# Optimization experiments

Measured on AMD Instinct MI355X. Metric: run time of the kernel, lower is better.

## Reference

```python
import jax, jax.numpy as jnp
import numpy as np

B, D, M_CONS = 512, 1024, 256
TOL = 0.01          # projection_tolerance
ROUNDS = 3
RHO0 = 3.0          # step
XRHO0 = 0.5         # forward() default xrho
FACTOR = 1.0
MAX_ITER = 30       # cap on the (originally unbounded) Dykstra while-loop


def setup_inputs() -> dict:
    key = jax.random.key(0)
    k1, k2, k3, k4, k5 = jax.random.split(key, 5)
    A = jax.random.normal(k1, (M_CONS, D), jnp.float32) / np.float32(np.sqrt(D))
    # feasible b so the polyhedron {Ax=b, x>=0} is nonempty and Dykstra converges
    x_feas = jax.nn.relu(jax.random.normal(k2, (D,), jnp.float32))
    b = A @ x_feas                                  # [M_CONS]
    AA = A.T @ jnp.linalg.inv(A @ A.T)              # [D, M_CONS], precomputed as in __init__
    c = jax.random.normal(k3, (B, D), jnp.float32)
    L = jax.random.normal(k4, (D, D), jnp.float32)
    Lam = 1.0 + 0.1 * jax.random.normal(k5, (D,), jnp.float32)
    return {"c": c, "A": A, "b": b, "AA": AA, "L": L, "Lam": Lam}


def reference(c, A, b, AA, L, Lam):
    # step matrix: L @ diag(Lam) @ inv(L)   (recomputed identically each round in torch)
    M = (L * Lam[None, :]) @ jnp.linalg.inv(L)      # [D, D]

    def proj(x):  # affine projection onto {Ax = b}: (x.T - AA @ (A x.T - b)).T
        return x - (x @ A.T - b[None, :]) @ AA.T    # [B, D]

    def project_pol(x0):  # Dykstra alternating projection onto {Ax=b} n {x>=0}
        def body(carry, _):
            x, p, q, y_out, done = carry
            y = proj(x + p)
            err = jnp.max(jax.nn.relu(-y))
            y_out = jnp.where(done, y_out, y)       # freeze output at first convergence
            xn = jax.nn.relu(y + q)
            pn = x + p - y
            qn = y + q - xn
            sel = lambda old, new: jnp.where(done, old, new)
            new_done = done | (err < TOL)
            return (sel(x, xn), sel(p, pn), sel(q, qn), y_out, new_done), None

        z = jnp.zeros_like(x0)
        init = (x0, z, z, x0, jnp.array(False))
        (xf, pf, qf, y_out, d), _ = jax.lax.scan(body, init, None, length=MAX_ITER)
        return y_out

    x = jnp.zeros_like(c)
    rho, xrho = RHO0, XRHO0
    for _ in range(ROUNDS):
        x = x - (xrho * (x @ M.T) + rho * c)
        x = project_pol(x)
        rho = rho * FACTOR
        xrho = xrho * FACTOR
    return x
```

## Files before the change

kernel.cpp:

```cpp
#include <hip/hip_runtime.h>

#define D      1024
#define BSZ    512
#define MC     256
#define NBK    64
#define NPAN   16
#define N_ROUNDS 3
#define MAXIT  30
#define TOLV   0.01f
#define RHOV   3.0f
#define XRHOV  0.5f
#define GRID   256
#define NGA    128
#define NGB    128

#define TS   0
#define QS   4096
#define US   8192
#define PART 9216
#define BS   13312
#define RED  13568
#define SMF  13600

struct KArgs {
  const float *c, *A, *b, *AA, *L, *Lam;
  float *yout, *F, *Ybuf, *Wm;
  float *t, *err, *At, *AAt;
  int *perm, *rmap;
  unsigned *slotsF, *slotsG;
};

__device__ __forceinline__ void fbar(unsigned* slots, int lid, int count, unsigned target) {
  __syncthreads();
  if (threadIdx.x == 0) {
    __builtin_amdgcn_fence(__ATOMIC_RELEASE, "agent");
    __hip_atomic_store(&slots[lid * 16], target, __ATOMIC_RELAXED, __HIP_MEMORY_SCOPE_AGENT);
  }
  for (int i = threadIdx.x; i < count; i += 256)
    while (__hip_atomic_load(&slots[i * 16], __ATOMIC_RELAXED, __HIP_MEMORY_SCOPE_AGENT) < target)
      __builtin_amdgcn_s_sleep(1);
  __builtin_amdgcn_fence(__ATOMIC_ACQUIRE, "agent");
  __syncthreads();
}

__device__ __forceinline__ void tile_fma(const float (*As)[68], const float (*Bs)[68],
                                         float acc[4][4], const int tx, const int ty) {
#pragma unroll 8
  for (int kk = 0; kk < 64; ++kk) {
    const float4 a4 = *(const float4*)(&As[kk][ty * 4]);
    const float4 b4 = *(const float4*)(&Bs[kk][tx * 4]);
    const float a0 = a4.x, a1 = a4.y, a2 = a4.z, a3 = a4.w;
    const float b0 = b4.x, b1 = b4.y, b2 = b4.z, b3 = b4.w;
    acc[0][0] = fmaf(a0, b0, acc[0][0]); acc[0][1] = fmaf(a0, b1, acc[0][1]);
    acc[0][2] = fmaf(a0, b2, acc[0][2]); acc[0][3] = fmaf(a0, b3, acc[0][3]);
    acc[1][0] = fmaf(a1, b0, acc[1][0]); acc[1][1] = fmaf(a1, b1, acc[1][1]);
    acc[1][2] = fmaf(a1, b2, acc[1][2]); acc[1][3] = fmaf(a1, b3, acc[1][3]);
    acc[2][0] = fmaf(a2, b0, acc[2][0]); acc[2][1] = fmaf(a2, b1, acc[2][1]);
    acc[2][2] = fmaf(a2, b2, acc[2][2]); acc[2][3] = fmaf(a2, b3, acc[2][3]);
    acc[3][0] = fmaf(a3, b0, acc[3][0]); acc[3][1] = fmaf(a3, b1, acc[3][1]);
    acc[3][2] = fmaf(a3, b2, acc[3][2]); acc[3][3] = fmaf(a3, b3, acc[3][3]);
  }
}

__device__ void ph_prep(float* sm, int vb, const float* L, const float* Lam,
                        float* F, float* Ybuf) {
  float (*tile)[65] = (float(*)[65])sm;
  const int bi = vb >> 4, bj = vb & 15;
  const int tx = threadIdx.x & 63, ty4 = threadIdx.x >> 6;
  const int i0 = bi * 64, j0 = bj * 64;
  for (int r = ty4; r < 64; r += 4) {
    const float v = L[(size_t)(i0 + r) * D + j0 + tx];
    F[(size_t)(i0 + r) * D + j0 + tx] = v;
    tile[r][tx] = v;
  }
  __syncthreads();
  for (int r = ty4; r < 64; r += 4) {
    const int j = j0 + r;
    Ybuf[(size_t)j * D + i0 + tx] = Lam[j] * tile[tx][r];
  }
  __syncthreads();
}

__device__ void ph_transpose(float* sm, const float* src, float* dst,
                             int srows, int scols, int tr, int tc) {
  float (*tile)[65] = (float(*)[65])sm;
  const int tx = threadIdx.x & 63, ty = threadIdx.x >> 6;
  for (int r = ty; r < 64; r += 4)
    tile[r][tx] = src[(size_t)(tr * 64 + r) * scols + tc * 64 + tx];
  __syncthreads();
  for (int r = ty; r < 64; r += 4)
    dst[(size_t)(tc * 64 + r) * srows + tr * 64 + tx] = tile[tx][r];
  __syncthreads();
}

__device__ void ph_lu_diag(float* sm, float* F, int* perm, int* rmap, int k) {
  float (*blk)[65] = (float(*)[65])sm;
  int* pr_sh = (int*)&sm[8960];
  int* rmp   = (int*)&sm[8964];
  const int tid = threadIdx.x;
  const int c0 = k * NBK;
  for (int e = tid; e < 4096; e += 256) {
    const int r = e >> 6, c = e & 63;
    blk[r][c] = F[(size_t)(c0 + r) * D + c0 + c];
  }
  if (tid < 64) rmp[tid] = tid;
  __syncthreads();
  for (int j = 0; j < 64; ++j) {
    if (tid < 64) {
      float v = (tid >= j) ? fabsf(blk[tid][j]) : -1.0f;
      int ridx = tid;
      for (int off = 32; off > 0; off >>= 1) {
        const float ov = __shfl_down(v, off);
        const int oi = __shfl_down(ridx, off);
        if (ov > v) { v = ov; ridx = oi; }
      }
      if (tid == 0) *pr_sh = ridx;
    }
    __syncthreads();
    const int pr = *pr_sh;
    if (pr != j) {
      if (tid < 64) { const float a = blk[j][tid], b = blk[pr][tid]; blk[j][tid] = b; blk[pr][tid] = a; }
      if (tid == 0) {
        int t = perm[c0 + j]; perm[c0 + j] = perm[c0 + pr]; perm[c0 + pr] = t;
        t = rmp[j]; rmp[j] = rmp[pr]; rmp[pr] = t;
      }
    }
    __syncthreads();
    const float inv = 1.0f / blk[j][j];
    const int r = tid >> 2, l4 = tid & 3;
    if (r > j) {
      const float lval = blk[r][j] * inv;
      if (l4 == 0) blk[r][j] = lval;
      for (int c = j + 1 + l4; c < 64; c += 4)
        blk[r][c] = fmaf(-lval, blk[j][c], blk[r][c]);
    }
    __syncthreads();
  }
  for (int e = tid; e < 4096; e += 256) {
    const int r = e >> 6, c = e & 63;
    F[(size_t)(c0 + r) * D + c0 + c] = blk[r][c];
  }
  if (tid < 64) rmap[tid] = rmp[tid];
  __syncthreads();
}

__device__ void ph_leftperm(float* sm, float* F, const int* rmap, int k, int chunk) {
  float (*tile)[65] = (float(*)[65])sm;
  int* rm = (int*)&sm[8960];
  const int tid = threadIdx.x;
  const int c0 = k * NBK;
  const int col0 = chunk * 64;
  if (tid < 64) rm[tid] = rmap[tid];
  __syncthreads();
  for (int e = tid; e < 4096; e += 256) {
    const int r = e >> 6, c = e & 63;
    tile[r][c] = F[(size_t)(c0 + rm[r]) * D + col0 + c];
  }
  __syncthreads();
  for (int e = tid; e < 4096; e += 256) {
    const int r = e >> 6, c = e & 63;
    F[(size_t)(c0 + r) * D + col0 + c] = tile[r][c];
  }
}

__device__ void ph_l21(float* sm, float* F, int k, int vb) {
  const int c0 = k * NBK;
  const int row0 = c0 + NBK;
  const int nrows = D - row0;
  float (*U)[65] = (float(*)[65])sm;
  const int tid = threadIdx.x;
  for (int e = tid; e < 4096; e += 256) { const int r = e >> 6, c = e & 63; U[r][c] = F[(size_t)(c0 + r) * D + c0 + c]; }
  __syncthreads();
  const int r = vb * 256 + tid;
  if (r >= nrows) return;
  float* Arow = &F[(size_t)(row0 + r) * D + c0];
  float x[64];
#pragma unroll
  for (int i = 0; i < 16; ++i) *(float4*)&x[i * 4] = *(const float4*)&Arow[i * 4];
#pragma unroll
  for (int jj = 0; jj < 64; ++jj) {
    float s0 = 0.f, s1 = 0.f, s2 = 0.f, s3 = 0.f;
#pragma unroll
    for (int i = 0; i + 3 < jj; i += 4) {
      s0 = fmaf(x[i], U[i][jj], s0);
      s1 = fmaf(x[i + 1], U[i + 1][jj], s1);
      s2 = fmaf(x[i + 2], U[i + 2][jj], s2);
      s3 = fmaf(x[i + 3], U[i + 3][jj], s3);
    }
#pragma unroll
    for (int i = (jj / 4) * 4; i < jj; ++i) s0 = fmaf(x[i], U[i][jj], s0);
    const float a = x[jj] - ((s0 + s1) + (s2 + s3));
    x[jj] = a / U[jj][jj];
  }
#pragma unroll
  for (int i = 0; i < 16; ++i) *(float4*)&Arow[i * 4] = *(const float4*)&x[i * 4];
}

__device__ void ph_trsm(float* sm, float* F, const int* rmap, int k, int vb) {
  const int c0 = k * NBK;
  const int colstart = c0 + NBK;
  const int ncols = D - colstart;
  float (*Lw)[65] = (float(*)[65])sm;
  int* rm = (int*)&sm[8960];
  const int tid = threadIdx.x;
  for (int e = tid; e < 4096; e += 256) { const int r = e >> 6, c = e & 63; Lw[r][c] = F[(size_t)(c0 + r) * D + c0 + c]; }
  if (tid < 64) rm[tid] = rmap[tid];
  __syncthreads();
  const int cidx = vb * 256 + tid;
  if (cidx >= ncols) return;
  const int col = colstart + cidx;
  float x[64];
#pragma unroll
  for (int i = 0; i < 64; ++i) x[i] = F[(size_t)(c0 + rm[i]) * D + col];
#pragma unroll
  for (int i = 0; i < 64; ++i) {
    float s0 = 0.f, s1 = 0.f, s2 = 0.f, s3 = 0.f;
#pragma unroll
    for (int j = 0; j + 3 < i; j += 4) {
      s0 = fmaf(Lw[i][j], x[j], s0);
      s1 = fmaf(Lw[i][j + 1], x[j + 1], s1);
      s2 = fmaf(Lw[i][j + 2], x[j + 2], s2);
      s3 = fmaf(Lw[i][j + 3], x[j + 3], s3);
    }
#pragma unroll
    for (int j = (i / 4) * 4; j < i; ++j) s0 = fmaf(Lw[i][j], x[j], s0);
    x[i] = x[i] - ((s0 + s1) + (s2 + s3));
  }
#pragma unroll
  for (int i = 0; i < 64; ++i) F[(size_t)(c0 + i) * D + col] = x[i];
}

__device__ void ph_gemm_nn(float* sm, float* F, int k, int vbx, int vby) {
  const int c0 = k * NBK;
  const int o = c0 + NBK;
  float (*As)[68] = (float(*)[68])sm;
  float (*Bs)[68] = (float(*)[68])&sm[4352];
  const int tid = threadIdx.x;
  const int cc0 = o + vbx * 64;
  const int r0 = o + vby * 64;
  for (int e = tid; e < 4096; e += 256) {
    const int r = e >> 6, c = e & 63;
    As[c][r] = F[(size_t)(r0 + r) * D + c0 + c];
    Bs[r][c] = F[(size_t)(c0 + r) * D + cc0 + c];
  }
  __syncthreads();
  float acc[4][4] = {};
  tile_fma(As, Bs, acc, tid & 15, tid >> 4);
  const int tx = tid & 15, ty = tid >> 4;
  for (int i = 0; i < 4; ++i)
    for (int j = 0; j < 4; ++j)
      F[(size_t)(r0 + ty * 4 + i) * D + cc0 + tx * 4 + j] -= acc[i][j];
  __syncthreads();
}

__device__ void ph_fsolve(float* sm, const float* F, float* Y, int k, int vb) {
  float (*T)[65] = (float(*)[65])sm;
  const int tid = threadIdx.x;
  const int c0 = k * NBK;
  for (int e = tid; e < 4096; e += 256) { const int r = e >> 6, c = e & 63; T[c][r] = F[(size_t)(c0 + r) * D + c0 + c]; }
  __syncthreads();
  const int col = vb * 256 + tid;
  float x[64];
#pragma unroll
  for (int i = 0; i < 64; ++i) x[i] = Y[(size_t)(c0 + i) * D + col];
#pragma unroll
  for (int i = 0; i < 64; ++i) {
    float s0 = 0.f, s1 = 0.f, s2 = 0.f, s3 = 0.f;
#pragma unroll
    for (int j = 0; j + 3 < i; j += 4) {
      s0 = fmaf(T[i][j], x[j], s0);
      s1 = fmaf(T[i][j + 1], x[j + 1], s1);
      s2 = fmaf(T[i][j + 2], x[j + 2], s2);
      s3 = fmaf(T[i][j + 3], x[j + 3], s3);
    }
#pragma unroll
    for (int j = (i / 4) * 4; j < i; ++j) s0 = fmaf(T[i][j], x[j], s0);
    const float a = x[i] - ((s0 + s1) + (s2 + s3));
    x[i] = a / T[i][i];
  }
#pragma unroll
  for (int i = 0; i < 64; ++i) Y[(size_t)(c0 + i) * D + col] = x[i];
  __syncthreads();
}

__device__ void ph_bsolve(float* sm, const float* F, float* Y, int k, int vb) {
  float (*T)[65] = (float(*)[65])sm;
  const int tid = threadIdx.x;
  const int c0 = k * NBK;
  for (int e = tid; e < 4096; e += 256) { const int r = e >> 6, c = e & 63; T[c][r] = F[(size_t)(c0 + r) * D + c0 + c]; }
  __syncthreads();
  const int col = vb * 256 + tid;
  float x[64];
#pragma unroll
  for (int i = 0; i < 64; ++i) x[i] = Y[(size_t)(c0 + i) * D + col];
#pragma unroll
  for (int i = 63; i >= 0; --i) {
    float s0 = 0.f, s1 = 0.f, s2 = 0.f, s3 = 0.f;
#pragma unroll
    for (int j = i + 1; j + 3 < 64; j += 4) {
      s0 = fmaf(T[i][j], x[j], s0);
      s1 = fmaf(T[i][j + 1], x[j + 1], s1);
      s2 = fmaf(T[i][j + 2], x[j + 2], s2);
      s3 = fmaf(T[i][j + 3], x[j + 3], s3);
    }
#pragma unroll
    for (int j = i + 1 + (((63 - i) / 4) * 4); j < 64; ++j) s0 = fmaf(T[i][j], x[j], s0);
    x[i] = x[i] - ((s0 + s1) + (s2 + s3));
  }
#pragma unroll
  for (int i = 0; i < 64; ++i) Y[(size_t)(c0 + i) * D + col] = x[i];
  __syncthreads();
}

__device__ void ph_tn(float* sm, const float* F, float* Y, int k, int rlo, int vbx, int vby) {
  const int c0 = k * NBK;
  float (*As)[68] = (float(*)[68])sm;
  float (*Bs)[68] = (float(*)[68])&sm[4352];
  const int tid = threadIdx.x;
  const int cc0 = vbx * 64;
  const int r0 = rlo + vby * 64;
  for (int e = tid; e < 4096; e += 256) {
    const int r = e >> 6, c = e & 63;
    As[r][c] = F[(size_t)(c0 + r) * D + r0 + c];
    Bs[r][c] = Y[(size_t)(c0 + r) * D + cc0 + c];
  }
  __syncthreads();
  float acc[4][4] = {};
  tile_fma(As, Bs, acc, tid & 15, tid >> 4);
  const int tx = tid & 15, ty = tid >> 4;
  for (int i = 0; i < 4; ++i)
    for (int j = 0; j < 4; ++j)
      Y[(size_t)(r0 + ty * 4 + i) * D + cc0 + tx * 4 + j] -= acc[i][j];
  __syncthreads();
}

__device__ void ph_scatter(const float* Y, float* Wm, const int* perm, int vb) {
  const int i = vb >> 2;
  const int c = (vb & 3) * 256 + threadIdx.x;
  Wm[(size_t)perm[i] * D + c] = Y[(size_t)i * D + c];
}

__device__ void ph_round(float* sm, const float* yout, const float* Wm, const float* cmat,
                         float* t, int vbx, int vby) {
  float (*As)[68] = (float(*)[68])sm;
  float (*Bs)[68] = (float(*)[68])&sm[4352];
  const int tid = threadIdx.x;
  const int i0 = vbx * 64;
  const int b0 = vby * 64;
  float acc[4][4] = {};
  for (int kb = 0; kb < D; kb += 64) {
    for (int e = tid; e < 4096; e += 256) {
      const int r = e >> 6, c = e & 63;
      As[c][r] = yout[(size_t)(b0 + r) * D + kb + c];
      Bs[r][c] = Wm[(size_t)(kb + r) * D + i0 + c];
    }
    __syncthreads();
    tile_fma(As, Bs, acc, tid & 15, tid >> 4);
    __syncthreads();
  }
  const int tx = tid & 15, ty = tid >> 4;
  for (int i = 0; i < 4; ++i)
    for (int j = 0; j < 4; ++j) {
      const int b = b0 + ty * 4 + i, col = i0 + tx * 4 + j;
      const float v = yout[(size_t)b * D + col] - XRHOV * acc[i][j] - RHOV * cmat[(size_t)b * D + col];
      t[(size_t)b * D + col] = v;
    }
  __syncthreads();
}

__device__ void dyk_state_init(float* sm, const KArgs& a, int r0) {
  float4* ts4 = (float4*)(sm + TS);
  float4* qs4 = (float4*)(sm + QS);
  const float4* t4 = (const float4*)(a.t + (size_t)r0 * D);
  for (int e = threadIdx.x; e < 1024; e += 256) {
    ts4[e] = t4[e];
    qs4[e] = make_float4(0.f, 0.f, 0.f, 0.f);
  }
  if (threadIdx.x < 256) sm[BS + threadIdx.x] = a.b[threadIdx.x];
  __syncthreads();
}

__device__ void dyk_iter(float* sm, const KArgs& a, int r0, int it, int base) {
  const int tid = threadIdx.x;
  float* ts = sm + TS;
  float* qs = sm + QS;
  float* us = sm + US;
  float* part = sm + PART;

  const int m4 = tid & 63, ks = tid >> 6;
  const float* AtB = a.At + (size_t)ks * 256 * MC + m4 * 4;
  float4 ua[4];
#pragma unroll
  for (int r = 0; r < 4; ++r) ua[r] = make_float4(0.f, 0.f, 0.f, 0.f);
  const int kb = ks * 256;
#pragma unroll 2
  for (int k4 = 0; k4 < 64; ++k4) {
    float t0[4], t1[4], t2[4], t3[4];
    *(float4*)t0 = *(const float4*)&ts[kb + k4 * 4];
    *(float4*)t1 = *(const float4*)&ts[1024 + kb + k4 * 4];
    *(float4*)t2 = *(const float4*)&ts[2048 + kb + k4 * 4];
    *(float4*)t3 = *(const float4*)&ts[3072 + kb + k4 * 4];
#pragma unroll
    for (int j = 0; j < 4; ++j) {
      const float4 av = *(const float4*)(AtB + (size_t)(k4 * 4 + j) * MC);
      ua[0].x = fmaf(t0[j], av.x, ua[0].x); ua[0].y = fmaf(t0[j], av.y, ua[0].y);
      ua[0].z = fmaf(t0[j], av.z, ua[0].z); ua[0].w = fmaf(t0[j], av.w, ua[0].w);
      ua[1].x = fmaf(t1[j], av.x, ua[1].x); ua[1].y = fmaf(t1[j], av.y, ua[1].y);
      ua[1].z = fmaf(t1[j], av.z, ua[1].z); ua[1].w = fmaf(t1[j], av.w, ua[1].w);
      ua[2].x = fmaf(t2[j], av.x, ua[2].x); ua[2].y = fmaf(t2[j], av.y, ua[2].y);
      ua[2].z = fmaf(t2[j], av.z, ua[2].z); ua[2].w = fmaf(t2[j], av.w, ua[2].w);
      ua[3].x = fmaf(t3[j], av.x, ua[3].x); ua[3].y = fmaf(t3[j], av.y, ua[3].y);
      ua[3].z = fmaf(t3[j], av.z, ua[3].z); ua[3].w = fmaf(t3[j], av.w, ua[3].w);
    }
  }
#pragma unroll
  for (int r = 0; r < 4; ++r) ((float4*)part)[(ks * 4 + r) * 64 + m4] = ua[r];
  __syncthreads();

  {
    const int m = tid;
#pragma unroll
    for (int r = 0; r < 4; ++r)
      us[r * 256 + m] = part[r * 256 + m] + part[1024 + r * 256 + m] +
                        part[2048 + r * 256 + m] + part[3072 + r * 256 + m] - sm[BS + m];
  }
  __syncthreads();

  float4 ya[4];
#pragma unroll
  for (int r = 0; r < 4; ++r) ya[r] = make_float4(0.f, 0.f, 0.f, 0.f);
  const float4* AAB = (const float4*)a.AAt;
#pragma unroll 2
  for (int mi = 0; mi < 64; ++mi) {
    float u0[4], u1[4], u2[4], u3[4];
    *(float4*)u0 = *(const float4*)&us[mi * 4];
    *(float4*)u1 = *(const float4*)&us[256 + mi * 4];
    *(float4*)u2 = *(const float4*)&us[512 + mi * 4];
    *(float4*)u3 = *(const float4*)&us[768 + mi * 4];
#pragma unroll
    for (int j = 0; j < 4; ++j) {
      const float4 w = AAB[(size_t)(mi * 4 + j) * (D / 4) + tid];
      ya[0].x = fmaf(u0[j], w.x, ya[0].x); ya[0].y = fmaf(u0[j], w.y, ya[0].y);
      ya[0].z = fmaf(u0[j], w.z, ya[0].z); ya[0].w = fmaf(u0[j], w.w, ya[0].w);
      ya[1].x = fmaf(u1[j], w.x, ya[1].x); ya[1].y = fmaf(u1[j], w.y, ya[1].y);
      ya[1].z = fmaf(u1[j], w.z, ya[1].z); ya[1].w = fmaf(u1[j], w.w, ya[1].w);
      ya[2].x = fmaf(u2[j], w.x, ya[2].x); ya[2].y = fmaf(u2[j], w.y, ya[2].y);
      ya[2].z = fmaf(u2[j], w.z, ya[2].z); ya[2].w = fmaf(u2[j], w.w, ya[2].w);
      ya[3].x = fmaf(u3[j], w.x, ya[3].x); ya[3].y = fmaf(u3[j], w.y, ya[3].y);
      ya[3].z = fmaf(u3[j], w.z, ya[3].z); ya[3].w = fmaf(u3[j], w.w, ya[3].w);
    }
  }

  float nmax = 0.f;
#pragma unroll
  for (int r = 0; r < 4; ++r) {
    const float4 tv = *(const float4*)&ts[r * 1024 + tid * 4];
    float4 y;
    y.x = tv.x - ya[r].x; y.y = tv.y - ya[r].y;
    y.z = tv.z - ya[r].z; y.w = tv.w - ya[r].w;
    ((float4*)a.yout)[(size_t)(r0 + r) * (D / 4) + tid] = y;
    const float4 qv = *(const float4*)&qs[r * 1024 + tid * 4];
    float4 tn, qn;
    { const float yq = y.x + qv.x, xn = fmaxf(yq, 0.f); tn.x = xn + (tv.x - y.x); qn.x = yq - xn; }
    { const float yq = y.y + qv.y, xn = fmaxf(yq, 0.f); tn.y = xn + (tv.y - y.y); qn.y = yq - xn; }
    { const float yq = y.z + qv.z, xn = fmaxf(yq, 0.f); tn.z = xn + (tv.z - y.z); qn.z = yq - xn; }
    { const float yq = y.w + qv.w, xn = fmaxf(yq, 0.f); tn.w = xn + (tv.w - y.w); qn.w = yq - xn; }
    *(float4*)&ts[r * 1024 + tid * 4] = tn;
    *(float4*)&qs[r * 1024 + tid * 4] = qn;
    nmax = fmaxf(nmax, -y.x); nmax = fmaxf(nmax, -y.y);
    nmax = fmaxf(nmax, -y.z); nmax = fmaxf(nmax, -y.w);
  }
#pragma unroll
  for (int off = 32; off > 0; off >>= 1) nmax = fmaxf(nmax, __shfl_down(nmax, off));
  if ((tid & 63) == 0) sm[RED + (tid >> 6)] = nmax;
  __syncthreads();
  if (tid == 0) {
    const float m = fmaxf(fmaxf(sm[RED], sm[RED + 1]), fmaxf(sm[RED + 2], sm[RED + 3]));
    atomicMax((int*)&a.err[base + it], __float_as_int(m));
  }
}

__device__ void dyk_round(float* sm, const KArgs& a, int bid, int base, unsigned& genG) {
  const int r0 = bid * 4;
  dyk_state_init(sm, a, r0);
  for (int it = 0; it < MAXIT; ++it) {
    dyk_iter(sm, a, r0, it, base);
    fbar(a.slotsG, bid, NGA, ++genG);
    const int eb = __hip_atomic_load((int*)&a.err[base + it], __ATOMIC_RELAXED,
                                     __HIP_MEMORY_SCOPE_AGENT);
    if (__int_as_float(eb) < TOLV) break;
  }
}

__global__ __launch_bounds__(256, 1) void mega(KArgs a) {
  __shared__ alignas(16) float sm[SMF];
  const int bid = blockIdx.x;
  const int tid = threadIdx.x;
  unsigned genF = 0, genG = 0;

  {
    const int gtid = bid * 256 + tid;
    for (int i = gtid; i < BSZ * D; i += GRID * 256) a.t[i] = -RHOV * a.c[i];
    if (gtid < D) a.perm[gtid] = gtid;
  }
  for (int vb = bid; vb < 384; vb += GRID) {
    if (vb < 256) ph_prep(sm, vb, a.L, a.Lam, a.F, a.Ybuf);
    else if (vb < 320) { const int tt = vb - 256; ph_transpose(sm, a.A, a.At, MC, D, tt & 3, tt >> 2); }
    else { const int tt = vb - 320; ph_transpose(sm, a.AA, a.AAt, D, MC, tt & 15, tt >> 4); }
  }
  fbar(a.slotsF, bid, GRID, ++genF);

  if (bid < NGA) {
    dyk_round(sm, a, bid, 0, genG);
    fbar(a.slotsF, bid, GRID, ++genF);
    for (int r = 1; r < N_ROUNDS; ++r) {
      ph_round(sm, a.yout, a.Wm, a.c, a.t, bid & 15, bid >> 4);
      fbar(a.slotsG, bid, NGA, ++genG);
      dyk_round(sm, a, bid, r * MAXIT, genG);
    }
  } else {
    unsigned* slotsB = a.slotsG + NGB * 16;
    const int vbid = bid - NGA;
    for (int k = 0; k < NPAN; ++k) {
      if (vbid == 0) ph_lu_diag(sm, a.F, a.perm, a.rmap, k);
      fbar(slotsB, vbid, NGB, ++genG);
      const int rem = D - (k + 1) * NBK;
      const int nvb = (rem > 0) ? (rem + 255) / 256 : 0;
      const int ntask = k + 2 * nvb;
      for (int vb = vbid; vb < ntask; vb += NGB) {
        if (vb < k) ph_leftperm(sm, a.F, a.rmap, k, vb);
        else if (vb < k + nvb) ph_l21(sm, a.F, k, vb - k);
        else ph_trsm(sm, a.F, a.rmap, k, vb - k - nvb);
      }
      fbar(slotsB, vbid, NGB, ++genG);
      if (rem > 0) {
        const int nt = rem / 64;
        for (int vb = vbid; vb < nt * nt; vb += NGB) ph_gemm_nn(sm, a.F, k, vb % nt, vb / nt);
        fbar(slotsB, vbid, NGB, ++genG);
      }
    }
    for (int k = 0; k < NPAN; ++k) {
      for (int vb = vbid; vb < 4; vb += NGB) ph_fsolve(sm, a.F, a.Ybuf, k, vb);
      fbar(slotsB, vbid, NGB, ++genG);
      const int rem = D - (k + 1) * NBK;
      if (rem > 0) {
        for (int vb = vbid; vb < 16 * (rem / 64); vb += NGB)
          ph_tn(sm, a.F, a.Ybuf, k, (k + 1) * NBK, vb & 15, vb >> 4);
        fbar(slotsB, vbid, NGB, ++genG);
      }
    }
    for (int k = NPAN - 1; k >= 0; --k) {
      for (int vb = vbid; vb < 4; vb += NGB) ph_bsolve(sm, a.F, a.Ybuf, k, vb);
      fbar(slotsB, vbid, NGB, ++genG);
      if (k > 0) {
        for (int vb = vbid; vb < 16 * k; vb += NGB)
          ph_tn(sm, a.F, a.Ybuf, k, 0, vb & 15, vb >> 4);
        fbar(slotsB, vbid, NGB, ++genG);
      }
    }
    for (int vb = vbid; vb < 4 * D; vb += NGB) ph_scatter(a.Ybuf, a.Wm, a.perm, vb);
    fbar(a.slotsF, bid, GRID, ++genF);
  }
}

extern "C" void kernel_launch(void* const* d_in, const int* in_sizes, int n_in,
                              void* d_out, int out_size, void* d_ws, size_t ws_size,
                              hipStream_t stream) {
  (void)in_sizes; (void)n_in; (void)out_size; (void)ws_size;
  KArgs a;
  a.c   = (const float*)d_in[0];
  a.A   = (const float*)d_in[1];
  a.b   = (const float*)d_in[2];
  a.AA  = (const float*)d_in[3];
  a.L   = (const float*)d_in[4];
  a.Lam = (const float*)d_in[5];
  a.yout = (float*)d_out;

  char* w = (char*)d_ws;
  a.slotsF = (unsigned*)w;
  a.slotsG = (unsigned*)(w + 16384);
  a.err    = (float*)(w + 32768);
  a.rmap   = (int*)(w + 33280);
  w += 36864;
  a.F    = (float*)w; w += (size_t)D * D * 4;
  a.Ybuf = (float*)w; w += (size_t)D * D * 4;
  a.Wm   = (float*)w; w += (size_t)D * D * 4;
  a.t    = (float*)w; w += (size_t)BSZ * D * 4;
  a.At   = (float*)w; w += (size_t)D * MC * 4;
  a.AAt  = (float*)w; w += (size_t)MC * D * 4;
  a.perm = (int*)w;   w += (size_t)D * 4;

  hipMemsetAsync(d_ws, 0, 36864, stream);
  mega<<<dim3(GRID), dim3(256), 0, stream>>>(a);
}
```

Baseline: 6.066 ms.

## Spread later Dykstra rounds over all blocks and replace barrier with per-block error flags

```diff
diff --git a/kernel.cpp b/kernel.cpp
--- a/kernel.cpp
+++ b/kernel.cpp
@@ -25,9 +25,9 @@
 struct KArgs {
   const float *c, *A, *b, *AA, *L, *Lam;
   float *yout, *F, *Ybuf, *Wm;
-  float *t, *err, *At, *AAt;
+  float *t, *At, *AAt;
   int *perm, *rmap;
-  unsigned *slotsF, *slotsG;
+  unsigned *slotsF, *slotsG, *errb;
 };
 
 __device__ __forceinline__ void fbar(unsigned* slots, int lid, int count, unsigned target) {
@@ -368,19 +368,21 @@
   __syncthreads();
 }
 
+template <int R>
 __device__ void dyk_state_init(float* sm, const KArgs& a, int r0) {
   float4* ts4 = (float4*)(sm + TS);
   float4* qs4 = (float4*)(sm + QS);
   const float4* t4 = (const float4*)(a.t + (size_t)r0 * D);
-  for (int e = threadIdx.x; e < 1024; e += 256) {
+  for (int e = threadIdx.x; e < R * 256; e += 256) {
     ts4[e] = t4[e];
     qs4[e] = make_float4(0.f, 0.f, 0.f, 0.f);
   }
-  if (threadIdx.x < 256) sm[BS + threadIdx.x] = a.b[threadIdx.x];
-  __syncthreads();
-}
-
-__device__ void dyk_iter(float* sm, const KArgs& a, int r0, int it, int base) {
+  sm[BS + threadIdx.x] = a.b[threadIdx.x];
+  __syncthreads();
+}
+
+template <int R>
+__device__ void dyk_iter(float* sm, const KArgs& a, int r0) {
   const int tid = threadIdx.x;
   float* ts = sm + TS;
   float* qs = sm + QS;
@@ -389,71 +391,65 @@
 
   const int m4 = tid & 63, ks = tid >> 6;
   const float* AtB = a.At + (size_t)ks * 256 * MC + m4 * 4;
-  float4 ua[4];
-#pragma unroll
-  for (int r = 0; r < 4; ++r) ua[r] = make_float4(0.f, 0.f, 0.f, 0.f);
+  float4 ua[R];
+#pragma unroll
+  for (int r = 0; r < R; ++r) ua[r] = make_float4(0.f, 0.f, 0.f, 0.f);
   const int kb = ks * 256;
 #pragma unroll 2
   for (int k4 = 0; k4 < 64; ++k4) {
-    float t0[4], t1[4], t2[4], t3[4];
-    *(float4*)t0 = *(const float4*)&ts[kb + k4 * 4];
-    *(float4*)t1 = *(const float4*)&ts[1024 + kb + k4 * 4];
-    *(float4*)t2 = *(const float4*)&ts[2048 + kb + k4 * 4];
-    *(float4*)t3 = *(const float4*)&ts[3072 + kb + k4 * 4];
+    float tr[R][4];
+#pragma unroll
+    for (int r = 0; r < R; ++r) *(float4*)tr[r] = *(const float4*)&ts[r * 1024 + kb + k4 * 4];
 #pragma unroll
     for (int j = 0; j < 4; ++j) {
       const float4 av = *(const float4*)(AtB + (size_t)(k4 * 4 + j) * MC);
-      ua[0].x = fmaf(t0[j], av.x, ua[0].x); ua[0].y = fmaf(t0[j], av.y, ua[0].y);
-      ua[0].z = fmaf(t0[j], av.z, ua[0].z); ua[0].w = fmaf(t0[j], av.w, ua[0].w);
-      ua[1].x = fmaf(t1[j], av.x, ua[1].x); ua[1].y = fmaf(t1[j], av.y, ua[1].y);
-      ua[1].z = fmaf(t1[j], av.z, ua[1].z); ua[1].w = fmaf(t1[j], av.w, ua[1].w);
-      ua[2].x = fmaf(t2[j], av.x, ua[2].x); ua[2].y = fmaf(t2[j], av.y, ua[2].y);
-      ua[2].z = fmaf(t2[j], av.z, ua[2].z); ua[2].w = fmaf(t2[j], av.w, ua[2].w);
-      ua[3].x = fmaf(t3[j], av.x, ua[3].x); ua[3].y = fmaf(t3[j], av.y, ua[3].y);
-      ua[3].z = fmaf(t3[j], av.z, ua[3].z); ua[3].w = fmaf(t3[j], av.w, ua[3].w);
-    }
-  }
-#pragma unroll
-  for (int r = 0; r < 4; ++r) ((float4*)part)[(ks * 4 + r) * 64 + m4] = ua[r];
+#pragma unroll
+      for (int r = 0; r < R; ++r) {
+        ua[r].x = fmaf(tr[r][j], av.x, ua[r].x);
+        ua[r].y = fmaf(tr[r][j], av.y, ua[r].y);
+        ua[r].z = fmaf(tr[r][j], av.z, ua[r].z);
+        ua[r].w = fmaf(tr[r][j], av.w, ua[r].w);
+      }
+    }
+  }
+#pragma unroll
+  for (int r = 0; r < R; ++r) ((float4*)part)[(ks * R + r) * 64 + m4] = ua[r];
   __syncthreads();
 
   {
     const int m = tid;
 #pragma unroll
-    for (int r = 0; r < 4; ++r)
-      us[r * 256 + m] = part[r * 256 + m] + part[1024 + r * 256 + m] +
-                        part[2048 + r * 256 + m] + part[3072 + r * 256 + m] - sm[BS + m];
-  }
-  __syncthreads();
-
-  float4 ya[4];
-#pragma unroll
-  for (int r = 0; r < 4; ++r) ya[r] = make_float4(0.f, 0.f, 0.f, 0.f);
+    for (int r = 0; r < R; ++r)
+      us[r * 256 + m] = part[(0 * R + r) * 256 + m] + part[(1 * R + r) * 256 + m] +
+                        part[(2 * R + r) * 256 + m] + part[(3 * R + r) * 256 + m] - sm[BS + m];
+  }
+  __syncthreads();
+
+  float4 ya[R];
+#pragma unroll
+  for (int r = 0; r < R; ++r) ya[r] = make_float4(0.f, 0.f, 0.f, 0.f);
   const float4* AAB = (const float4*)a.AAt;
 #pragma unroll 2
   for (int mi = 0; mi < 64; ++mi) {
-    float u0[4], u1[4], u2[4], u3[4];
-    *(float4*)u0 = *(const float4*)&us[mi * 4];
-    *(float4*)u1 = *(const float4*)&us[256 + mi * 4];
-    *(float4*)u2 = *(const float4*)&us[512 + mi * 4];
-    *(float4*)u3 = *(const float4*)&us[768 + mi * 4];
+    float ur[R][4];
+#pragma unroll
+    for (int r = 0; r < R; ++r) *(float4*)ur[r] = *(const float4*)&us[r * 256 + mi * 4];
 #pragma unroll
     for (int j = 0; j < 4; ++j) {
       const float4 w = AAB[(size_t)(mi * 4 + j) * (D / 4) + tid];
-      ya[0].x = fmaf(u0[j], w.x, ya[0].x); ya[0].y = fmaf(u0[j], w.y, ya[0].y);
-      ya[0].z = fmaf(u0[j], w.z, ya[0].z); ya[0].w = fmaf(u0[j], w.w, ya[0].w);
-      ya[1].x = fmaf(u1[j], w.x, ya[1].x); ya[1].y = fmaf(u1[j], w.y, ya[1].y);
-      ya[1].z = fmaf(u1[j], w.z, ya[1].z); ya[1].w = fmaf(u1[j], w.w, ya[1].w);
-      ya[2].x = fmaf(u2[j], w.x, ya[2].x); ya[2].y = fmaf(u2[j], w.y, ya[2].y);
-      ya[2].z = fmaf(u2[j], w.z, ya[2].z); ya[2].w = fmaf(u2[j], w.w, ya[2].w);
-      ya[3].x = fmaf(u3[j], w.x, ya[3].x); ya[3].y = fmaf(u3[j], w.y, ya[3].y);
-      ya[3].z = fmaf(u3[j], w.z, ya[3].z); ya[3].w = fmaf(u3[j], w.w, ya[3].w);
+#pragma unroll
+      for (int r = 0; r < R; ++r) {
+        ya[r].x = fmaf(ur[r][j], w.x, ya[r].x);
+        ya[r].y = fmaf(ur[r][j], w.y, ya[r].y);
+        ya[r].z = fmaf(ur[r][j], w.z, ya[r].z);
+        ya[r].w = fmaf(ur[r][j], w.w, ya[r].w);
+      }
     }
   }
 
   float nmax = 0.f;
 #pragma unroll
-  for (int r = 0; r < 4; ++r) {
+  for (int r = 0; r < R; ++r) {
     const float4 tv = *(const float4*)&ts[r * 1024 + tid * 4];
     float4 y;
     y.x = tv.x - ya[r].x; y.y = tv.y - ya[r].y;
@@ -474,21 +470,39 @@
   for (int off = 32; off > 0; off >>= 1) nmax = fmaxf(nmax, __shfl_down(nmax, off));
   if ((tid & 63) == 0) sm[RED + (tid >> 6)] = nmax;
   __syncthreads();
-  if (tid == 0) {
-    const float m = fmaxf(fmaxf(sm[RED], sm[RED + 1]), fmaxf(sm[RED + 2], sm[RED + 3]));
-    atomicMax((int*)&a.err[base + it], __float_as_int(m));
-  }
-}
-
-__device__ void dyk_round(float* sm, const KArgs& a, int bid, int base, unsigned& genG) {
-  const int r0 = bid * 4;
-  dyk_state_init(sm, a, r0);
+}
+
+template <int R>
+__device__ void dyk_round(float* sm, const KArgs& a, int bid, int nblk, int base) {
+  const int r0 = bid * R;
+  dyk_state_init<R>(sm, a, r0);
   for (int it = 0; it < MAXIT; ++it) {
-    dyk_iter(sm, a, r0, it, base);
-    fbar(a.slotsG, bid, NGA, ++genG);
-    const int eb = __hip_atomic_load((int*)&a.err[base + it], __ATOMIC_RELAXED,
-                                     __HIP_MEMORY_SCOPE_AGENT);
-    if (__int_as_float(eb) < TOLV) break;
+    dyk_iter<R>(sm, a, r0);
+    if (threadIdx.x == 0) {
+      const float bmax = fmaxf(fmaxf(sm[RED], sm[RED + 1]), fmaxf(sm[RED + 2], sm[RED + 3]));
+      __hip_atomic_store(&a.errb[(size_t)(base + it) * GRID + bid],
+                         __float_as_uint(bmax) | 0x80000000u,
+                         __ATOMIC_RELAXED, __HIP_MEMORY_SCOPE_AGENT);
+    }
+    float v = 0.f;
+    if (threadIdx.x < nblk) {
+      unsigned u = __hip_atomic_load(&a.errb[(size_t)(base + it) * GRID + threadIdx.x],
+                                     __ATOMIC_RELAXED, __HIP_MEMORY_SCOPE_AGENT);
+      while (!(u & 0x80000000u)) {
+        __builtin_amdgcn_s_sleep(1);
+        u = __hip_atomic_load(&a.errb[(size_t)(base + it) * GRID + threadIdx.x],
+                              __ATOMIC_RELAXED, __HIP_MEMORY_SCOPE_AGENT);
+      }
+      v = __uint_as_float(u & 0x7FFFFFFFu);
+    }
+#pragma unroll
+    for (int off = 32; off > 0; off >>= 1) v = fmaxf(v, __shfl_down(v, off));
+    __syncthreads();
+    if ((threadIdx.x & 63) == 0) sm[RED + (threadIdx.x >> 6)] = v;
+    __syncthreads();
+    const float gmax = fmaxf(fmaxf(sm[RED], sm[RED + 1]), fmaxf(sm[RED + 2], sm[RED + 3]));
+    __syncthreads();
+    if (gmax < TOLV) break;
   }
 }
 
@@ -511,13 +525,8 @@
   fbar(a.slotsF, bid, GRID, ++genF);
 
   if (bid < NGA) {
-    dyk_round(sm, a, bid, 0, genG);
+    dyk_round<4>(sm, a, bid, NGA, 0);
     fbar(a.slotsF, bid, GRID, ++genF);
-    for (int r = 1; r < N_ROUNDS; ++r) {
-      ph_round(sm, a.yout, a.Wm, a.c, a.t, bid & 15, bid >> 4);
-      fbar(a.slotsG, bid, NGA, ++genG);
-      dyk_round(sm, a, bid, r * MAXIT, genG);
-    }
   } else {
     unsigned* slotsB = a.slotsG + NGB * 16;
     const int vbid = bid - NGA;
@@ -561,6 +570,14 @@
     for (int vb = vbid; vb < 4 * D; vb += NGB) ph_scatter(a.Ybuf, a.Wm, a.perm, vb);
     fbar(a.slotsF, bid, GRID, ++genF);
   }
+
+  for (int r = 1; r < N_ROUNDS; ++r) {
+    if (bid < 128) ph_round(sm, a.yout, a.Wm, a.c, a.t, bid & 15, bid >> 4);
+    fbar(a.slotsF, bid, GRID, ++genF);
+    dyk_round<2>(sm, a, bid, GRID, r * MAXIT);
+    if (r + 1 < N_ROUNDS)
+      fbar(a.slotsF, bid, GRID, ++genF);
+  }
 }
 
 extern "C" void kernel_launch(void* const* d_in, const int* in_sizes, int n_in,
@@ -579,9 +596,9 @@
   char* w = (char*)d_ws;
   a.slotsF = (unsigned*)w;
   a.slotsG = (unsigned*)(w + 16384);
-  a.err    = (float*)(w + 32768);
-  a.rmap   = (int*)(w + 33280);
-  w += 36864;
+  a.errb   = (unsigned*)(w + 32768);
+  a.rmap   = (int*)(w + 124928);
+  w += 131072;
   a.F    = (float*)w; w += (size_t)D * D * 4;
   a.Ybuf = (float*)w; w += (size_t)D * D * 4;
   a.Wm   = (float*)w; w += (size_t)D * D * 4;
@@ -590,6 +607,6 @@
   a.AAt  = (float*)w; w += (size_t)MC * D * 4;
   a.perm = (int*)w;   w += (size_t)D * 4;
 
-  hipMemsetAsync(d_ws, 0, 36864, stream);
+  hipMemsetAsync(d_ws, 0, 131072, stream);
   mega<<<dim3(GRID), dim3(256), 0, stream>>>(a);
 }
```

Result: faster. 5.864 ms (-3.3%).
